# Performance work log

Hardware: AMD Instinct MI355X
Metric: run time of the kernel (lower is better)

Reference implementation:

```python
import jax, jax.numpy as jnp
import numpy as np

EPS = 1e-5

def _layernorm(x, w, b):
    mu = jnp.mean(x, axis=-1, keepdims=True)
    var = jnp.var(x, axis=-1, keepdims=True)
    return (x - mu) * jax.lax.rsqrt(var + EPS) * w + b

def setup_inputs() -> dict:
    key = jax.random.key(0)
    ks = jax.random.split(key, 9)
    b, s, dim = 4, 4096, 2048
    m, n, dim_ctx = 8, 64, 1024
    heads, dim_head = 8, 64
    inner = heads * dim_head
    x = jax.random.normal(ks[0], (b, s, dim), dtype=jnp.float32)
    context = jax.random.normal(ks[1], (b, m, n, dim_ctx), dtype=jnp.float32)
    media_locations = jax.random.randint(ks[2], (b, s), 0, m, dtype=jnp.int64)
    scale = 0.02
    norm_w = jnp.ones((dim,), jnp.float32)
    norm_b = jnp.zeros((dim,), jnp.float32)
    normc_w = jnp.ones((dim_ctx,), jnp.float32)
    normc_b = jnp.zeros((dim_ctx,), jnp.float32)
    Wq = jax.random.normal(ks[3], (dim, inner), jnp.float32) * scale
    Wkv = jax.random.normal(ks[4], (dim_ctx, 2 * inner), jnp.float32) * scale
    Wout = jax.random.normal(ks[5], (inner, dim), jnp.float32) * scale
    return {"x": x, "context": context, "media_locations": media_locations,
            "norm_w": norm_w, "norm_b": norm_b, "normc_w": normc_w, "normc_b": normc_b,
            "Wq": Wq, "Wkv": Wkv, "Wout": Wout}

def reference(x, context, media_locations, norm_w, norm_b, normc_w, normc_b, Wq, Wkv, Wout):
    heads, dim_head = 8, 64
    b, m, n, dc = context.shape
    scale = dim_head ** -0.5
    xn = _layernorm(x, norm_w, norm_b)                       # [b,s,dim]
    ctx = _layernorm(context.reshape(b, m * n, dc), normc_w, normc_b)  # [b,mn,dc]
    q = xn @ Wq                                              # [b,s,inner]
    kv = ctx @ Wkv                                           # [b,mn,2*inner]
    k, v = jnp.split(kv, 2, axis=-1)
    def to_heads(t):
        return t.reshape(t.shape[0], t.shape[1], heads, dim_head).transpose(0, 2, 1, 3)
    q, k, v = to_heads(q), to_heads(k), to_heads(v)          # [b,h,*,d]
    sim = jnp.einsum('bhid,bhjd->bhij', q, k) * scale        # [b,h,s,mn]
    # image-causal mask: kv token j belongs to image j//n; query i may only
    # attend to image media_locations[b,i] (negative index => all masked)
    j_img = jnp.arange(m * n) // n                           # [mn]
    allowed = (media_locations[:, :, None] == j_img[None, None, :]) & (media_locations[:, :, None] >= 0)
    sim = jnp.where(allowed[:, None, :, :], sim, -jnp.inf)
    attn = jax.nn.softmax(sim, axis=-1)
    out = jnp.einsum('bhij,bhjd->bhid', attn, v)             # [b,h,s,d]
    out = out.transpose(0, 2, 1, 3).reshape(b, x.shape[1], heads * dim_head)
    return out @ Wout
```

## Files before the change

### kernel.cpp

```cpp
#include <hip/hip_runtime.h>

typedef unsigned short u16;
typedef unsigned int u32;
typedef __attribute__((ext_vector_type(8))) short short8;
typedef __attribute__((ext_vector_type(4))) short short4_t;
typedef __attribute__((ext_vector_type(4))) float f32x4;

__device__ __forceinline__ float bf2f(u16 u){ return __uint_as_float(((u32)u)<<16); }
__device__ __forceinline__ u16 f2bf(float f){ u32 x = __float_as_uint(f); return (u16)((x + 0x7FFFu + ((x>>16)&1u)) >> 16); }

#define OFF_FLAG   ((size_t)0)
#define OFF_COUNTS ((size_t)256)
#define OFF_LISTS  ((size_t)4096)
#define OFF_XN     ((size_t)(1<<20))
#define OFF_CTXN   (OFF_XN    + (size_t)67108864)
#define OFF_WQT    (OFF_CTXN  + (size_t)4194304)
#define OFF_WKVT   (OFF_WQT   + (size_t)2097152)
#define OFF_WOUTT  (OFF_WKVT  + (size_t)2097152)
#define OFF_Q      (OFF_WOUTT + (size_t)2097152)
#define OFF_KV     (OFF_Q     + (size_t)16777216)
#define OFF_ATTN   (OFF_KV    + (size_t)4194304)
#define OFF_VT     (OFF_ATTN  + (size_t)16777216)
#define WS_NEEDED  (OFF_VT    + (size_t)2097152)

__global__ __launch_bounds__(256) void ln_x(const float* __restrict__ x, const float* __restrict__ w,
                                            const float* __restrict__ b, u16* __restrict__ out){
  constexpr int D = 2048, VEC = 8;
  int row = blockIdx.x;
  const float* xr = x + (size_t)row*D;
  int tid = threadIdx.x;
  float v[VEC];
  #pragma unroll
  for (int i=0;i<VEC;i+=4){
    f32x4 f = *(const f32x4*)(xr + tid*VEC + i);
    v[i]=f[0]; v[i+1]=f[1]; v[i+2]=f[2]; v[i+3]=f[3];
  }
  float s=0.f, sq=0.f;
  #pragma unroll
  for (int i=0;i<VEC;++i){ s += v[i]; sq += v[i]*v[i]; }
  #pragma unroll
  for (int off=32;off;off>>=1){ s += __shfl_xor(s,off,64); sq += __shfl_xor(sq,off,64); }
  __shared__ float red[8];
  int lane = tid&63, wid = tid>>6;
  if (lane==0){ red[wid]=s; red[4+wid]=sq; }
  __syncthreads();
  s  = red[0]+red[1]+red[2]+red[3];
  sq = red[4]+red[5]+red[6]+red[7];
  float mu = s/(float)D;
  float var = sq/(float)D - mu*mu;
  float rs = rsqrtf(var + 1e-5f);
  u16 o[VEC];
  #pragma unroll
  for (int i=0;i<VEC;i+=4){
    f32x4 wv = *(const f32x4*)(w + tid*VEC + i);
    f32x4 bv = *(const f32x4*)(b + tid*VEC + i);
    #pragma unroll
    for (int u=0;u<4;++u) o[i+u] = f2bf((v[i+u]-mu)*rs*wv[u] + bv[u]);
  }
  *(short8*)(out + (size_t)row*D + tid*8) = *(short8*)o;
}

__global__ __launch_bounds__(256) void ctx_prep(const float* __restrict__ ctx, const float* __restrict__ ncw,
                                                const float* __restrict__ ncb, u16* __restrict__ ctxn,
                                                const float* __restrict__ Wq, const float* __restrict__ Wkv,
                                                const float* __restrict__ Wout, u16* __restrict__ WqT,
                                                u16* __restrict__ WkvT, u16* __restrict__ WoutT,
                                                const int* __restrict__ ml32, int* __restrict__ flag,
                                                int* __restrict__ counts){
  int id = blockIdx.x, tid = threadIdx.x;
  __shared__ float red[8];
  __shared__ float t[32][33];
  __shared__ int nz;
  if (id < 2048){
    constexpr int D = 1024;
    const float* xr = ctx + (size_t)id*D;
    f32x4 f = *(const f32x4*)(xr + tid*4);
    float s = f[0]+f[1]+f[2]+f[3];
    float sq = f[0]*f[0]+f[1]*f[1]+f[2]*f[2]+f[3]*f[3];
    #pragma unroll
    for (int off=32;off;off>>=1){ s += __shfl_xor(s,off,64); sq += __shfl_xor(sq,off,64); }
    int lane = tid&63, wid = tid>>6;
    if (lane==0){ red[wid]=s; red[4+wid]=sq; }
    __syncthreads();
    s  = red[0]+red[1]+red[2]+red[3];
    sq = red[4]+red[5]+red[6]+red[7];
    float mu = s/(float)D;
    float var = sq/(float)D - mu*mu;
    float rs = rsqrtf(var + 1e-5f);
    f32x4 wv = *(const f32x4*)(ncw + tid*4);
    f32x4 bv = *(const f32x4*)(ncb + tid*4);
    u16 o[4];
    #pragma unroll
    for (int u=0;u<4;++u) o[u] = f2bf((f[u]-mu)*rs*wv[u] + bv[u]);
    *(short4_t*)(ctxn + (size_t)id*D + tid*4) = *(short4_t*)o;
  } else if (id < 5120){
    int wid2 = id - 2048;
    const float* in; u16* out; int K, N, tile, tx_n;
    if (wid2 < 1024)      { in=Wq;   out=WqT;   K=2048; N=512;  tile=wid2;      tx_n=16; }
    else if (wid2 < 2048) { in=Wkv;  out=WkvT;  K=1024; N=1024; tile=wid2-1024; tx_n=32; }
    else                  { in=Wout; out=WoutT; K=512;  N=2048; tile=wid2-2048; tx_n=64; }
    int n0 = (tile % tx_n)*32, k0 = (tile / tx_n)*32;
    int tx = tid & 31, ty = tid >> 5;
    #pragma unroll
    for (int r=0;r<32;r+=8) t[ty+r][tx] = in[(size_t)(k0+ty+r)*N + n0+tx];
    __syncthreads();
    #pragma unroll
    for (int r=0;r<32;r+=8) out[(size_t)(n0+ty+r)*K + k0+tx] = f2bf(t[tx][ty+r]);
  } else {
    if (tid < 32) counts[tid] = 0;
    if (tid == 0) nz = 0;
    __syncthreads();
    if (tid < 128 && ml32[2*tid+1] != 0) atomicAdd(&nz, 1);
    __syncthreads();
    if (tid == 0) flag[0] = (nz == 0) ? 1 : 0;
  }
}

template<int MODE>
__device__ __forceinline__ void gemm_body(u16 (*lds)[2][128*32],
                                          const u16* __restrict__ A, const u16* __restrict__ B,
                                          void* __restrict__ Cv, int M, int N, int K, int wg0, int nwg){
  int tid = threadIdx.x, lane = tid&63, wid = tid>>6;
  int nbn = N>>7;
  int wg = wg0;
  int cpx = nwg>>3;
  wg = (wg&7)*cpx + (wg>>3);
  int brow = wg/nbn, bcol = wg%nbn;

  auto stage = [&](int buf, int kt){
    #pragma unroll
    for (int i=0;i<2;++i){
      int cb = i*256 + wid*64;
      int c  = cb + lane;
      int row = c>>2, kc = c&3;
      const u16* ga = A + (size_t)(brow*128+row)*K + kt*32 + kc*8;
      __builtin_amdgcn_global_load_lds((const __attribute__((address_space(1))) u32*)ga,
          (__attribute__((address_space(3))) u32*)&lds[buf][0][cb*8], 16, 0, 0);
      const u16* gb = B + (size_t)(bcol*128+row)*K + kt*32 + kc*8;
      __builtin_amdgcn_global_load_lds((const __attribute__((address_space(1))) u32*)gb,
          (__attribute__((address_space(3))) u32*)&lds[buf][1][cb*8], 16, 0, 0);
    }
  };

  int wm = wid>>1, wn = wid&1;
  f32x4 acc[4][4] = {};
  int nkt = K>>5;
  stage(0,0);
  __syncthreads();
  for (int kt=0; kt<nkt; ++kt){
    int cur = kt&1;
    if (kt+1<nkt) stage(cur^1, kt+1);
    short8 af[4], bfr[4];
    int r = lane&15, kq = lane>>4;
    #pragma unroll
    for (int mi=0;mi<4;++mi) af[mi]  = *(const short8*)&lds[cur][0][(wm*64+mi*16+r)*32 + kq*8];
    #pragma unroll
    for (int ni=0;ni<4;++ni) bfr[ni] = *(const short8*)&lds[cur][1][(wn*64+ni*16+r)*32 + kq*8];
    #pragma unroll
    for (int mi=0;mi<4;++mi)
      #pragma unroll
      for (int ni=0;ni<4;++ni)
        acc[mi][ni] = __builtin_amdgcn_mfma_f32_16x16x32_bf16(af[mi], bfr[ni], acc[mi][ni], 0,0,0);
    __syncthreads();
  }
  int r4 = (lane>>4)*4, cc = lane&15;
  #pragma unroll
  for (int mi=0;mi<4;++mi)
    #pragma unroll
    for (int ni=0;ni<4;++ni)
      #pragma unroll
      for (int rr=0;rr<4;++rr){
        int row = brow*128 + wm*64 + mi*16 + r4 + rr;
        int col = bcol*128 + wn*64 + ni*16 + cc;
        float val = acc[mi][ni][rr];
        if (MODE==2) val *= 0.125f;
        if (MODE)  ((u16*)Cv)[(size_t)row*N+col] = f2bf(val);
        else       ((float*)Cv)[(size_t)row*N+col] = val;
      }
}

__global__ __launch_bounds__(256) void gemm_out(const u16* __restrict__ A, const u16* __restrict__ B,
                                                float* __restrict__ C){
  __shared__ __align__(16) u16 lds[2][2][128*32];
  gemm_body<0>(lds, A, B, C, 16384, 2048, 512, blockIdx.x, gridDim.x);
}

__global__ __launch_bounds__(256) void gemm_qkv(const u16* __restrict__ xn, const u16* __restrict__ WqT,
                                                u16* __restrict__ qbuf, const u16* __restrict__ ctxn,
                                                const u16* __restrict__ WkvT, u16* __restrict__ kvbuf){
  __shared__ __align__(16) u16 lds[2][2][128*32];
  if (blockIdx.x < 512) gemm_body<2>(lds, xn,   WqT,  qbuf,  16384, 512,  2048, blockIdx.x,     512);
  else                  gemm_body<1>(lds, ctxn, WkvT, kvbuf, 2048,  1024, 1024, blockIdx.x-512, 128);
}

__global__ __launch_bounds__(256) void tv_bucket(const u16* __restrict__ kvb, u16* __restrict__ vt,
                                                 const int* __restrict__ ml32, const int* __restrict__ flag,
                                                 int* __restrict__ counts, int* __restrict__ lists){
  int h = blockIdx.x, bl = blockIdx.y;
  int tid = threadIdx.x;
  int bid = bl*8 + h;
  __shared__ int lc[32], lbase[32];
  __shared__ u16 t[64][72];
  if (bid < 64){
    if (tid < 32) lc[tid] = 0;
    __syncthreads();
    int i = bid*256 + tid;
    int loc = flag[0] ? ml32[2*i] : ml32[i];
    int blk = (i>>12)*8 + loc;
    int lpos = atomicAdd(&lc[blk], 1);
    __syncthreads();
    if (tid < 32 && lc[tid] > 0) lbase[tid] = atomicAdd(&counts[tid], lc[tid]);
    __syncthreads();
    lists[blk*4096 + lbase[blk] + lpos] = i & 4095;
    __syncthreads();
  }
  const u16* src = kvb + (size_t)(bl*64)*1024 + 512 + h*64;
  #pragma unroll
  for (int i=0;i<2;++i){
    int idx = i*2048 + tid*8;
    int key = idx>>6, d = idx&63;
    *(short8*)&t[key][d] = *(const short8*)(src + (size_t)key*1024 + d);
  }
  __syncthreads();
  u16* dst = vt + (size_t)(bl*8+h)*4096;
  #pragma unroll
  for (int i=0;i<2;++i){
    int idx = i*2048 + tid*8;
    int d = idx>>6, k0 = idx&63;
    u16 tmp[8];
    #pragma unroll
    for (int u=0;u<8;++u) tmp[u] = t[k0+u][d];
    *(short8*)(dst + d*64 + k0) = *(short8*)tmp;
  }
}

__global__ __launch_bounds__(512) void attn_mfma5(const u16* __restrict__ qb, const u16* __restrict__ kvb,
                                                  const u16* __restrict__ vt, u16* __restrict__ ob,
                                                  const int* __restrict__ counts, const int* __restrict__ lists){
  int bl = blockIdx.y, chunk = blockIdx.x;
  int cnt = counts[bl];
  int q0 = chunk*32;
  if (q0 >= cnt) return;
  int b = bl>>3, loc = bl&7;
  int tid = threadIdx.x, lane = tid&63, h = tid>>6;
  __shared__ u16 qs[32][520];
  int r = lane&15, g = lane>>4;

  const u16* kbase = kvb + (size_t)(b*512 + loc*64)*1024 + h*64;
  short8 kfr[4][2];
  #pragma unroll
  for (int nt=0;nt<4;++nt){
    const u16* krow = kbase + (size_t)(nt*16 + r)*1024;
    kfr[nt][0] = *(const short8*)(krow + g*8);
    kfr[nt][1] = *(const short8*)(krow + 32 + g*8);
  }
  const u16* vbase = vt + (size_t)(bl*8 + h)*4096;
  short8 vf[2][4];
  #pragma unroll
  for (int nt=0;nt<4;++nt){
    const u16* vrow = vbase + (size_t)(nt*16 + r)*64;
    vf[0][nt] = *(const short8*)(vrow + g*8);
    vf[1][nt] = *(const short8*)(vrow + 32 + g*8);
  }

  const u16* qbase = qb + (size_t)(b*4096)*512;
  #pragma unroll
  for (int p=0;p<4;++p){
    int c = p*512 + tid;
    int row = c>>6, cc = c&63;
    int qq = (q0 + row < cnt) ? lists[bl*4096 + q0 + row] : -1;
    if (qq >= 0)
      *(short8*)&qs[row][cc*8] = *(const short8*)(qbase + (size_t)qq*512 + cc*8);
  }
  __syncthreads();

  short8 qf[2][2];
  #pragma unroll
  for (int mt=0;mt<2;++mt){
    qf[mt][0] = *(const short8*)&qs[mt*16+r][h*64 + g*8];
    qf[mt][1] = *(const short8*)&qs[mt*16+r][h*64 + 32 + g*8];
  }

  f32x4 acc[2][4] = {};
  #pragma unroll
  for (int mt=0;mt<2;++mt)
    #pragma unroll
    for (int nt=0;nt<4;++nt){
      acc[mt][nt] = __builtin_amdgcn_mfma_f32_16x16x32_bf16(qf[mt][0], kfr[nt][0], acc[mt][nt], 0,0,0);
      acc[mt][nt] = __builtin_amdgcn_mfma_f32_16x16x32_bf16(qf[mt][1], kfr[nt][1], acc[mt][nt], 0,0,0);
    }

  #pragma unroll
  for (int mt=0;mt<2;++mt){
    #pragma unroll
    for (int rr=0;rr<4;++rr){
      float m = fmaxf(fmaxf(acc[mt][0][rr], acc[mt][1][rr]), fmaxf(acc[mt][2][rr], acc[mt][3][rr]));
      #pragma unroll
      for (int off=1;off<16;off<<=1) m = fmaxf(m, __shfl_xor(m, off));
      float e0 = __expf(acc[mt][0][rr]-m), e1 = __expf(acc[mt][1][rr]-m);
      float e2 = __expf(acc[mt][2][rr]-m), e3 = __expf(acc[mt][3][rr]-m);
      float sum = (e0+e1)+(e2+e3);
      #pragma unroll
      for (int off=1;off<16;off<<=1) sum += __shfl_xor(sum, off);
      float rs = 1.0f/sum;
      int row = mt*16 + g*4 + rr;
      qs[row][h*64 +  0 + r] = f2bf(e0*rs);
      qs[row][h*64 + 16 + r] = f2bf(e1*rs);
      qs[row][h*64 + 32 + r] = f2bf(e2*rs);
      qs[row][h*64 + 48 + r] = f2bf(e3*rs);
    }
  }

  f32x4 oacc[2][4] = {};
  #pragma unroll
  for (int mt=0;mt<2;++mt){
    short8 pa0 = *(const short8*)&qs[mt*16 + r][h*64 + g*8];
    short8 pa1 = *(const short8*)&qs[mt*16 + r][h*64 + 32 + g*8];
    #pragma unroll
    for (int nt=0;nt<4;++nt){
      oacc[mt][nt] = __builtin_amdgcn_mfma_f32_16x16x32_bf16(pa0, vf[0][nt], oacc[mt][nt], 0,0,0);
      oacc[mt][nt] = __builtin_amdgcn_mfma_f32_16x16x32_bf16(pa1, vf[1][nt], oacc[mt][nt], 0,0,0);
    }
  }

  #pragma unroll
  for (int mt=0;mt<2;++mt)
    #pragma unroll
    for (int rr=0;rr<4;++rr){
      int row = mt*16 + g*4 + rr;
      #pragma unroll
      for (int nt=0;nt<4;++nt)
        qs[row][h*64 + nt*16 + r] = f2bf(oacc[mt][nt][rr]);
    }
  __syncthreads();

  #pragma unroll
  for (int p=0;p<4;++p){
    int c = p*512 + tid;
    int row = c>>6, cc = c&63;
    int qq = (q0 + row < cnt) ? lists[bl*4096 + q0 + row] : -1;
    if (qq >= 0)
      *(short8*)(ob + ((size_t)(b*4096) + qq)*512 + cc*8) = *(const short8*)&qs[row][cc*8];
  }
}

extern "C" void kernel_launch(void* const* d_in, const int* in_sizes, int n_in,
                              void* d_out, int out_size, void* d_ws, size_t ws_size,
                              hipStream_t stream) {
  const float* x    = (const float*)d_in[0];
  const float* ctx  = (const float*)d_in[1];
  const int*   ml   = (const int*)d_in[2];
  const float* nw   = (const float*)d_in[3];
  const float* nb   = (const float*)d_in[4];
  const float* ncw  = (const float*)d_in[5];
  const float* ncb  = (const float*)d_in[6];
  const float* Wq   = (const float*)d_in[7];
  const float* Wkv  = (const float*)d_in[8];
  const float* Wout = (const float*)d_in[9];
  float* out = (float*)d_out;
  char* ws = (char*)d_ws;
  if (ws_size < WS_NEEDED) return;

  int* flag   = (int*)(ws + OFF_FLAG);
  int* counts = (int*)(ws + OFF_COUNTS);
  int* lists  = (int*)(ws + OFF_LISTS);
  u16* xn     = (u16*)(ws + OFF_XN);
  u16* ctxn   = (u16*)(ws + OFF_CTXN);
  u16* WqT    = (u16*)(ws + OFF_WQT);
  u16* WkvT   = (u16*)(ws + OFF_WKVT);
  u16* WoutT  = (u16*)(ws + OFF_WOUTT);
  u16* qbuf   = (u16*)(ws + OFF_Q);
  u16* kvbuf  = (u16*)(ws + OFF_KV);
  u16* attn_o = (u16*)(ws + OFF_ATTN);
  u16* vtbuf  = (u16*)(ws + OFF_VT);

  ln_x<<<16384,256,0,stream>>>(x, nw, nb, xn);
  ctx_prep<<<5121,256,0,stream>>>(ctx, ncw, ncb, ctxn, Wq, Wkv, Wout, WqT, WkvT, WoutT, ml, flag, counts);
  gemm_qkv<<<640,256,0,stream>>>(xn, WqT, qbuf, ctxn, WkvT, kvbuf);
  tv_bucket<<<dim3(8,32),256,0,stream>>>(kvbuf, vtbuf, ml, flag, counts, lists);
  attn_mfma5<<<dim3(128,32),512,0,stream>>>(qbuf, kvbuf, vtbuf, attn_o, counts, lists);
  gemm_out<<<2048,256,0,stream>>>(attn_o, WoutT, out);
}
```

Baseline: 198.0 us.

## Merge prep kernels, fuse V-transpose and bucketing into QKV GEMM, add MFMA priority

Combines the x layernorm and context/weight prep into one launch and removes the separate tv_bucket kernel. The KV GEMM epilogue now writes V directly in transposed per-head layout, and the bucketing blocks are appended to the QKV GEMM grid. s_setprio hints are added around the attention MFMA sections. The goal is fewer launches and less traffic, at the cost of scattered 2-byte stores in the V epilogue and bucketing possibly running concurrently with the GEMM.

```diff
diff --git a/kernel.cpp b/kernel.cpp
--- a/kernel.cpp
+++ b/kernel.cpp
@@ -23,44 +23,9 @@
 #define OFF_VT     (OFF_ATTN  + (size_t)16777216)
 #define WS_NEEDED  (OFF_VT    + (size_t)2097152)
 
-__global__ __launch_bounds__(256) void ln_x(const float* __restrict__ x, const float* __restrict__ w,
-                                            const float* __restrict__ b, u16* __restrict__ out){
-  constexpr int D = 2048, VEC = 8;
-  int row = blockIdx.x;
-  const float* xr = x + (size_t)row*D;
-  int tid = threadIdx.x;
-  float v[VEC];
-  #pragma unroll
-  for (int i=0;i<VEC;i+=4){
-    f32x4 f = *(const f32x4*)(xr + tid*VEC + i);
-    v[i]=f[0]; v[i+1]=f[1]; v[i+2]=f[2]; v[i+3]=f[3];
-  }
-  float s=0.f, sq=0.f;
-  #pragma unroll
-  for (int i=0;i<VEC;++i){ s += v[i]; sq += v[i]*v[i]; }
-  #pragma unroll
-  for (int off=32;off;off>>=1){ s += __shfl_xor(s,off,64); sq += __shfl_xor(sq,off,64); }
-  __shared__ float red[8];
-  int lane = tid&63, wid = tid>>6;
-  if (lane==0){ red[wid]=s; red[4+wid]=sq; }
-  __syncthreads();
-  s  = red[0]+red[1]+red[2]+red[3];
-  sq = red[4]+red[5]+red[6]+red[7];
-  float mu = s/(float)D;
-  float var = sq/(float)D - mu*mu;
-  float rs = rsqrtf(var + 1e-5f);
-  u16 o[VEC];
-  #pragma unroll
-  for (int i=0;i<VEC;i+=4){
-    f32x4 wv = *(const f32x4*)(w + tid*VEC + i);
-    f32x4 bv = *(const f32x4*)(b + tid*VEC + i);
-    #pragma unroll
-    for (int u=0;u<4;++u) o[i+u] = f2bf((v[i+u]-mu)*rs*wv[u] + bv[u]);
-  }
-  *(short8*)(out + (size_t)row*D + tid*8) = *(short8*)o;
-}
-
-__global__ __launch_bounds__(256) void ctx_prep(const float* __restrict__ ctx, const float* __restrict__ ncw,
+__global__ __launch_bounds__(256) void prep_all(const float* __restrict__ x, const float* __restrict__ nw,
+                                                const float* __restrict__ nb, u16* __restrict__ xn,
+                                                const float* __restrict__ ctx, const float* __restrict__ ncw,
                                                 const float* __restrict__ ncb, u16* __restrict__ ctxn,
                                                 const float* __restrict__ Wq, const float* __restrict__ Wkv,
                                                 const float* __restrict__ Wout, u16* __restrict__ WqT,
@@ -71,9 +36,41 @@
   __shared__ float red[8];
   __shared__ float t[32][33];
   __shared__ int nz;
-  if (id < 2048){
+  if (id < 16384){
+    constexpr int D = 2048, VEC = 8;
+    const float* xr = x + (size_t)id*D;
+    float v[VEC];
+    #pragma unroll
+    for (int i=0;i<VEC;i+=4){
+      f32x4 f = *(const f32x4*)(xr + tid*VEC + i);
+      v[i]=f[0]; v[i+1]=f[1]; v[i+2]=f[2]; v[i+3]=f[3];
+    }
+    float s=0.f, sq=0.f;
+    #pragma unroll
+    for (int i=0;i<VEC;++i){ s += v[i]; sq += v[i]*v[i]; }
+    #pragma unroll
+    for (int off=32;off;off>>=1){ s += __shfl_xor(s,off,64); sq += __shfl_xor(sq,off,64); }
+    int lane = tid&63, wid = tid>>6;
+    if (lane==0){ red[wid]=s; red[4+wid]=sq; }
+    __syncthreads();
+    s  = red[0]+red[1]+red[2]+red[3];
+    sq = red[4]+red[5]+red[6]+red[7];
+    float mu = s/(float)D;
+    float var = sq/(float)D - mu*mu;
+    float rs = rsqrtf(var + 1e-5f);
+    u16 o[VEC];
+    #pragma unroll
+    for (int i=0;i<VEC;i+=4){
+      f32x4 wv = *(const f32x4*)(nw + tid*VEC + i);
+      f32x4 bv = *(const f32x4*)(nb + tid*VEC + i);
+      #pragma unroll
+      for (int u=0;u<4;++u) o[i+u] = f2bf((v[i+u]-mu)*rs*wv[u] + bv[u]);
+    }
+    *(short8*)(xn + (size_t)id*D + tid*8) = *(short8*)o;
+  } else if (id < 18432){
     constexpr int D = 1024;
-    const float* xr = ctx + (size_t)id*D;
+    int row = id - 16384;
+    const float* xr = ctx + (size_t)row*D;
     f32x4 f = *(const f32x4*)(xr + tid*4);
     float s = f[0]+f[1]+f[2]+f[3];
     float sq = f[0]*f[0]+f[1]*f[1]+f[2]*f[2]+f[3]*f[3];
@@ -92,9 +89,9 @@
     u16 o[4];
     #pragma unroll
     for (int u=0;u<4;++u) o[u] = f2bf((f[u]-mu)*rs*wv[u] + bv[u]);
-    *(short4_t*)(ctxn + (size_t)id*D + tid*4) = *(short4_t*)o;
-  } else if (id < 5120){
-    int wid2 = id - 2048;
+    *(short4_t*)(ctxn + (size_t)row*D + tid*4) = *(short4_t*)o;
+  } else if (id < 21504){
+    int wid2 = id - 18432;
     const float* in; u16* out; int K, N, tile, tx_n;
     if (wid2 < 1024)      { in=Wq;   out=WqT;   K=2048; N=512;  tile=wid2;      tx_n=16; }
     else if (wid2 < 2048) { in=Wkv;  out=WkvT;  K=1024; N=1024; tile=wid2-1024; tx_n=32; }
@@ -119,7 +116,8 @@
 template<int MODE>
 __device__ __forceinline__ void gemm_body(u16 (*lds)[2][128*32],
                                           const u16* __restrict__ A, const u16* __restrict__ B,
-                                          void* __restrict__ Cv, int M, int N, int K, int wg0, int nwg){
+                                          void* __restrict__ Cv, int M, int N, int K, int wg0, int nwg,
+                                          u16* __restrict__ vtp){
   int tid = threadIdx.x, lane = tid&63, wid = tid>>6;
   int nbn = N>>7;
   int wg = wg0;
@@ -165,43 +163,41 @@
   }
   int r4 = (lane>>4)*4, cc = lane&15;
   #pragma unroll
-  for (int mi=0;mi<4;++mi)
-    #pragma unroll
-    for (int ni=0;ni<4;++ni)
+  for (int mi=0;mi<4;++mi){
+    int rowb = brow*128 + wm*64 + mi*16 + r4;
+    #pragma unroll
+    for (int ni=0;ni<4;++ni){
+      int col = bcol*128 + wn*64 + ni*16 + cc;
       #pragma unroll
       for (int rr=0;rr<4;++rr){
-        int row = brow*128 + wm*64 + mi*16 + r4 + rr;
-        int col = bcol*128 + wn*64 + ni*16 + cc;
+        int row = rowb + rr;
         float val = acc[mi][ni][rr];
-        if (MODE==2) val *= 0.125f;
-        if (MODE)  ((u16*)Cv)[(size_t)row*N+col] = f2bf(val);
-        else       ((float*)Cv)[(size_t)row*N+col] = val;
+        if (MODE==0)      ((float*)Cv)[(size_t)row*N+col] = val;
+        else if (MODE==2) ((u16*)Cv)[(size_t)row*N+col] = f2bf(val*0.125f);
+        else {
+          if (col < 512)  ((u16*)Cv)[(size_t)row*N+col] = f2bf(val);
+          else {
+            int hv = (col-512)>>6, d = (col-512)&63;
+            vtp[(size_t)((row>>6)*8 + hv)*4096 + d*64 + (row&63)] = f2bf(val);
+          }
+        }
       }
-}
-
-__global__ __launch_bounds__(256) void gemm_out(const u16* __restrict__ A, const u16* __restrict__ B,
-                                                float* __restrict__ C){
-  __shared__ __align__(16) u16 lds[2][2][128*32];
-  gemm_body<0>(lds, A, B, C, 16384, 2048, 512, blockIdx.x, gridDim.x);
+    }
+  }
 }
 
 __global__ __launch_bounds__(256) void gemm_qkv(const u16* __restrict__ xn, const u16* __restrict__ WqT,
                                                 u16* __restrict__ qbuf, const u16* __restrict__ ctxn,
-                                                const u16* __restrict__ WkvT, u16* __restrict__ kvbuf){
+                                                const u16* __restrict__ WkvT, u16* __restrict__ kvbuf,
+                                                u16* __restrict__ vtbuf,
+                                                const int* __restrict__ ml32, const int* __restrict__ flag,
+                                                int* __restrict__ counts, int* __restrict__ lists){
   __shared__ __align__(16) u16 lds[2][2][128*32];
-  if (blockIdx.x < 512) gemm_body<2>(lds, xn,   WqT,  qbuf,  16384, 512,  2048, blockIdx.x,     512);
-  else                  gemm_body<1>(lds, ctxn, WkvT, kvbuf, 2048,  1024, 1024, blockIdx.x-512, 128);
-}
-
-__global__ __launch_bounds__(256) void tv_bucket(const u16* __restrict__ kvb, u16* __restrict__ vt,
-                                                 const int* __restrict__ ml32, const int* __restrict__ flag,
-                                                 int* __restrict__ counts, int* __restrict__ lists){
-  int h = blockIdx.x, bl = blockIdx.y;
-  int tid = threadIdx.x;
-  int bid = bl*8 + h;
   __shared__ int lc[32], lbase[32];
-  __shared__ u16 t[64][72];
-  if (bid < 64){
+  if (blockIdx.x < 512)      gemm_body<2>(lds, xn,   WqT,  qbuf,  16384, 512,  2048, blockIdx.x,     512, nullptr);
+  else if (blockIdx.x < 640) gemm_body<3>(lds, ctxn, WkvT, kvbuf, 2048,  1024, 1024, blockIdx.x-512, 128, vtbuf);
+  else {
+    int bid = blockIdx.x - 640, tid = threadIdx.x;
     if (tid < 32) lc[tid] = 0;
     __syncthreads();
     int i = bid*256 + tid;
@@ -212,26 +208,13 @@
     if (tid < 32 && lc[tid] > 0) lbase[tid] = atomicAdd(&counts[tid], lc[tid]);
     __syncthreads();
     lists[blk*4096 + lbase[blk] + lpos] = i & 4095;
-    __syncthreads();
-  }
-  const u16* src = kvb + (size_t)(bl*64)*1024 + 512 + h*64;
-  #pragma unroll
-  for (int i=0;i<2;++i){
-    int idx = i*2048 + tid*8;
-    int key = idx>>6, d = idx&63;
-    *(short8*)&t[key][d] = *(const short8*)(src + (size_t)key*1024 + d);
-  }
-  __syncthreads();
-  u16* dst = vt + (size_t)(bl*8+h)*4096;
-  #pragma unroll
-  for (int i=0;i<2;++i){
-    int idx = i*2048 + tid*8;
-    int d = idx>>6, k0 = idx&63;
-    u16 tmp[8];
-    #pragma unroll
-    for (int u=0;u<8;++u) tmp[u] = t[k0+u][d];
-    *(short8*)(dst + d*64 + k0) = *(short8*)tmp;
-  }
+  }
+}
+
+__global__ __launch_bounds__(256) void gemm_out(const u16* __restrict__ A, const u16* __restrict__ B,
+                                                float* __restrict__ C){
+  __shared__ __align__(16) u16 lds[2][2][128*32];
+  gemm_body<0>(lds, A, B, C, 16384, 2048, 512, blockIdx.x, gridDim.x, nullptr);
 }
 
 __global__ __launch_bounds__(512) void attn_mfma5(const u16* __restrict__ qb, const u16* __restrict__ kvb,
@@ -282,6 +265,7 @@
   }
 
   f32x4 acc[2][4] = {};
+  __builtin_amdgcn_s_setprio(1);
   #pragma unroll
   for (int mt=0;mt<2;++mt)
     #pragma unroll
@@ -289,6 +273,7 @@
       acc[mt][nt] = __builtin_amdgcn_mfma_f32_16x16x32_bf16(qf[mt][0], kfr[nt][0], acc[mt][nt], 0,0,0);
       acc[mt][nt] = __builtin_amdgcn_mfma_f32_16x16x32_bf16(qf[mt][1], kfr[nt][1], acc[mt][nt], 0,0,0);
     }
+  __builtin_amdgcn_s_setprio(0);
 
   #pragma unroll
   for (int mt=0;mt<2;++mt){
@@ -316,11 +301,13 @@
   for (int mt=0;mt<2;++mt){
     short8 pa0 = *(const short8*)&qs[mt*16 + r][h*64 + g*8];
     short8 pa1 = *(const short8*)&qs[mt*16 + r][h*64 + 32 + g*8];
+    __builtin_amdgcn_s_setprio(1);
     #pragma unroll
     for (int nt=0;nt<4;++nt){
       oacc[mt][nt] = __builtin_amdgcn_mfma_f32_16x16x32_bf16(pa0, vf[0][nt], oacc[mt][nt], 0,0,0);
       oacc[mt][nt] = __builtin_amdgcn_mfma_f32_16x16x32_bf16(pa1, vf[1][nt], oacc[mt][nt], 0,0,0);
     }
+    __builtin_amdgcn_s_setprio(0);
   }
 
   #pragma unroll
@@ -374,10 +361,9 @@
   u16* attn_o = (u16*)(ws + OFF_ATTN);
   u16* vtbuf  = (u16*)(ws + OFF_VT);
 
-  ln_x<<<16384,256,0,stream>>>(x, nw, nb, xn);
-  ctx_prep<<<5121,256,0,stream>>>(ctx, ncw, ncb, ctxn, Wq, Wkv, Wout, WqT, WkvT, WoutT, ml, flag, counts);
-  gemm_qkv<<<640,256,0,stream>>>(xn, WqT, qbuf, ctxn, WkvT, kvbuf);
-  tv_bucket<<<dim3(8,32),256,0,stream>>>(kvbuf, vtbuf, ml, flag, counts, lists);
+  prep_all<<<21505,256,0,stream>>>(x, nw, nb, xn, ctx, ncw, ncb, ctxn,
+                                   Wq, Wkv, Wout, WqT, WkvT, WoutT, ml, flag, counts);
+  gemm_qkv<<<704,256,0,stream>>>(xn, WqT, qbuf, ctxn, WkvT, kvbuf, vtbuf, ml, flag, counts, lists);
   attn_mfma5<<<dim3(128,32),512,0,stream>>>(qbuf, kvbuf, vtbuf, attn_o, counts, lists);
   gemm_out<<<2048,256,0,stream>>>(attn_o, WoutT, out);
 }
```

Result: no change. 200.0 us (+1.0%).
